# Performance work log

Hardware: AMD Instinct MI355X
Metric: run time of the kernel (lower is better)

The kernel has to match this reference:

```python
import jax, jax.numpy as jnp
import numpy as np

D_MODEL = 768
N_HEADS = 12
D_K = D_MODEL // N_HEADS


def setup_inputs() -> dict:
    key = jax.random.key(0)
    kq, kk, kv, kwq, kbq, kwo, kbo = jax.random.split(key, 7)
    B, S = 1, 4096
    s = 1.0 / np.sqrt(D_MODEL)
    return {
        "q": jax.random.normal(kq, (B, S, D_MODEL), jnp.float32),
        "k": jax.random.normal(kk, (B, S, D_MODEL), jnp.float32),
        "v": jax.random.normal(kv, (B, S, D_MODEL), jnp.float32),
        # nn.Linear weights stored as [out, in]; note the original forward
        # uses W_q for Q, K, AND V (W_k/W_v are never used), so only W_q and
        # W_o are materialized here.
        "Wq": jax.random.uniform(kwq, (D_MODEL, D_MODEL), jnp.float32, -s, s),
        "bq": jax.random.uniform(kbq, (D_MODEL,), jnp.float32, -s, s),
        "Wo": jax.random.uniform(kwo, (D_MODEL, D_MODEL), jnp.float32, -s, s),
        "bo": jax.random.uniform(kbo, (D_MODEL,), jnp.float32, -s, s),
    }


def _split_heads(x):  # [B,S,D] -> [B,H,S,Dk]
    B, S, _ = x.shape
    return x.reshape(B, S, N_HEADS, D_K).transpose(0, 2, 1, 3)


def reference(q, k, v, Wq, bq, Wo, bo):
    # Faithful to source: same W_q projection applied to q, k, v.
    Q = _split_heads(q @ Wq.T + bq)
    K = _split_heads(k @ Wq.T + bq)
    V = _split_heads(v @ Wq.T + bq)
    scale = 1.0 / np.sqrt(D_K).astype(np.float32)
    scores = jnp.einsum("bhqd,bhkd->bhqk", Q, K) * scale  # [B,H,S,S]
    probs = jax.nn.softmax(scores, axis=-1)
    atten = jnp.einsum("bhqk,bhkd->bhqd", probs, V)
    B, _, S, _ = atten.shape
    concat = atten.transpose(0, 2, 1, 3).reshape(B, S, D_MODEL)
    return concat @ Wo.T + bo
```

## Files before the change

### kernel.cpp

```cpp
#include <hip/hip_runtime.h>
#include <stdint.h>
#include <math.h>


#define SQ 4096
#define DM 768
#define NH 12

typedef float f32x4 __attribute__((ext_vector_type(4)));
typedef short bf16x8 __attribute__((ext_vector_type(8)));
typedef unsigned int u32x4 __attribute__((ext_vector_type(4)));
typedef unsigned int u32x2 __attribute__((ext_vector_type(2)));
typedef unsigned short ushort_t;

#define MFMA32(a, b, c) __builtin_amdgcn_mfma_f32_16x16x32_bf16((a), (b), (c), 0, 0, 0)

static __device__ __forceinline__ ushort_t f2bf(float f) {
    unsigned int u = __builtin_bit_cast(unsigned int, f);
    u += 0x7fffu + ((u >> 16) & 1u);
    return (ushort_t)(u >> 16);
}

static __device__ __forceinline__ unsigned int cvt_pk_bf16(float a, float b) {
    unsigned int d;
    asm("v_cvt_pk_bf16_f32 %0, %1, %2" : "=v"(d) : "v"(a), "v"(b));
    return d;
}

static __device__ __forceinline__ float exp2_hw(float x) {
    float r;
    asm("v_exp_f32 %0, %1" : "=v"(r) : "v"(x));
    return r;
}

static __device__ __forceinline__ void gload16(const ushort_t* g, ushort_t* l) {
    __builtin_amdgcn_global_load_lds(
        reinterpret_cast<const __attribute__((address_space(1))) unsigned int*>(
            reinterpret_cast<uintptr_t>(g)),
        reinterpret_cast<__attribute__((address_space(3))) unsigned int*>(
            reinterpret_cast<uintptr_t>(l)),
        16, 0, 0);
}

#define WAITV8 do { asm volatile("s_waitcnt vmcnt(8)" ::: "memory"); \
                    __builtin_amdgcn_sched_barrier(0); } while (0)
#define WAITV4 do { asm volatile("s_waitcnt vmcnt(4)" ::: "memory"); \
                    __builtin_amdgcn_sched_barrier(0); } while (0)
#define WAITV0 do { asm volatile("s_waitcnt vmcnt(0)" ::: "memory"); \
                    __builtin_amdgcn_sched_barrier(0); } while (0)
#define WAITLGKM0 do { asm volatile("s_waitcnt lgkmcnt(0)" ::: "memory"); \
                       __builtin_amdgcn_sched_barrier(0); } while (0)

__global__ __launch_bounds__(256) void cvt_all(
    const float* __restrict__ q, const float* __restrict__ k,
    const float* __restrict__ v, const float* __restrict__ Wq,
    const float* __restrict__ Wo, ushort_t* __restrict__ xb,
    ushort_t* __restrict__ wqb, ushort_t* __restrict__ wob) {
    const int NE4 = (SQ * DM) / 4;
    const int NW4 = (DM * DM) / 4;
    int i = blockIdx.x * 256 + threadIdx.x;
    const float* src;
    ushort_t* dst;
    if (i < NE4) { src = q; dst = xb; }
    else if (i < 2 * NE4) { src = k; dst = xb + SQ * DM; i -= NE4; }
    else if (i < 3 * NE4) { src = v; dst = xb + 2 * SQ * DM; i -= 2 * NE4; }
    else if (i < 3 * NE4 + NW4) { src = Wq; dst = wqb; i -= 3 * NE4; }
    else if (i < 3 * NE4 + 2 * NW4) { src = Wo; dst = wob; i -= 3 * NE4 + NW4; }
    else return;
    float4 x = reinterpret_cast<const float4*>(src)[i];
    ushort4 o;
    o.x = f2bf(x.x); o.y = f2bf(x.y); o.z = f2bf(x.z); o.w = f2bf(x.w);
    reinterpret_cast<ushort4*>(dst)[i] = o;
}

__global__ __launch_bounds__(256) void gemm_qkv(
    const ushort_t* __restrict__ xb, const ushort_t* __restrict__ wqb,
    const float* __restrict__ bq, ushort_t* __restrict__ proj,
    ushort_t* __restrict__ vt) {
    __shared__ __align__(16) ushort_t lsA[128 * 64];
    __shared__ __align__(16) ushort_t lsB[128 * 64];
    const int tid = threadIdx.x;
    const int lane = tid & 63;
    const int w = tid >> 6;
    const int wm = w >> 1, wn = w & 1;
    const int g = lane >> 4, li = lane & 15;
    const bool isV = blockIdx.x >= 384;
    const ushort_t* A;
    const ushort_t* B;
    int bm, bn;
    if (!isV) {
        A = xb; B = wqb;
        bm = blockIdx.x / 6; bn = blockIdx.x % 6;
    } else {
        A = wqb; B = xb + 2 * SQ * DM;
        const int b2 = blockIdx.x - 384;
        bm = b2 / 32; bn = b2 % 32;
    }
    const int arow = bm * 128, brow = bn * 128;
    const int sr = lane >> 3;
    const int sc = ((lane & 7) ^ sr) * 8;

    f32x4 acc[4][4] = {};

    for (int kt = 0; kt < 12; ++kt) {
        const int k0 = kt * 64;
        __syncthreads();
#pragma unroll
        for (int c = 0; c < 4; ++c) {
            const int chunk = w * 4 + c;
            const int r = chunk * 8 + sr;
            gload16(A + (size_t)(arow + r) * DM + k0 + sc, lsA + chunk * 512);
            gload16(B + (size_t)(brow + r) * DM + k0 + sc, lsB + chunk * 512);
        }
        __syncthreads();

        bf16x8 af[4][2];
#pragma unroll
        for (int mf = 0; mf < 4; ++mf) {
            const int row = wm * 64 + mf * 16 + li;
#pragma unroll
            for (int ks = 0; ks < 2; ++ks)
                af[mf][ks] = *reinterpret_cast<const bf16x8*>(
                    lsA + row * 64 + ((ks * 32 + g * 8) ^ ((li & 7) << 3)));
        }
#pragma unroll
        for (int nf = 0; nf < 4; ++nf) {
            const int row = wn * 64 + nf * 16 + li;
            bf16x8 b0 = *reinterpret_cast<const bf16x8*>(
                lsB + row * 64 + ((g * 8) ^ ((li & 7) << 3)));
            bf16x8 b1 = *reinterpret_cast<const bf16x8*>(
                lsB + row * 64 + ((32 + g * 8) ^ ((li & 7) << 3)));
#pragma unroll
            for (int mf = 0; mf < 4; ++mf) {
                acc[mf][nf] = MFMA32(af[mf][0], b0, acc[mf][nf]);
                acc[mf][nf] = MFMA32(af[mf][1], b1, acc[mf][nf]);
            }
        }
    }

    if (!isV) {
        const float qscale = (arow < 4096) ? 0.18033688011112042f : 1.0f;
#pragma unroll
        for (int nf = 0; nf < 4; ++nf) {
            const int col = brow + wn * 64 + nf * 16 + li;
            const float bv = bq[col];
#pragma unroll
            for (int mf = 0; mf < 4; ++mf) {
                const int row0 = arow + wm * 64 + mf * 16 + g * 4;
#pragma unroll
                for (int r = 0; r < 4; ++r)
                    proj[(size_t)(row0 + r) * DM + col] = f2bf((acc[mf][nf][r] + bv) * qscale);
            }
        }
    } else {
        float bv[4][4];
#pragma unroll
        for (int mf = 0; mf < 4; ++mf)
#pragma unroll
            for (int r = 0; r < 4; ++r)
                bv[mf][r] = bq[arow + wm * 64 + mf * 16 + g * 4 + r];
        const int xg = (g & 1) << 3;
#pragma unroll
        for (int nf = 0; nf < 4; ++nf) {
            const int j = brow + wn * 64 + nf * 16 + li;
            const int pos = j ^ xg;
#pragma unroll
            for (int mf = 0; mf < 4; ++mf) {
                const int row0 = arow + wm * 64 + mf * 16 + g * 4;
#pragma unroll
                for (int r = 0; r < 4; ++r)
                    vt[(size_t)(row0 + r) * SQ + pos] = f2bf(acc[mf][nf][r] + bv[mf][r]);
            }
        }
    }
}

__global__ __launch_bounds__(256) void gemm_out(
    const ushort_t* __restrict__ cc, const ushort_t* __restrict__ wob,
    const float* __restrict__ bo, float* __restrict__ outf) {
    __shared__ __align__(16) ushort_t lsA[128 * 64];
    __shared__ __align__(16) ushort_t lsB[128 * 64];
    const int tid = threadIdx.x;
    const int lane = tid & 63;
    const int w = tid >> 6;
    const int wm = w >> 1, wn = w & 1;
    const int g = lane >> 4, li = lane & 15;
    const int bm = blockIdx.x / 6, bn = blockIdx.x % 6;
    const int arow = bm * 128, brow = bn * 128;
    const int sr = lane >> 3;
    const int sc = ((lane & 7) ^ sr) * 8;

    f32x4 acc[4][4] = {};

    for (int kt = 0; kt < 12; ++kt) {
        const int k0 = kt * 64;
        __syncthreads();
#pragma unroll
        for (int c = 0; c < 4; ++c) {
            const int chunk = w * 4 + c;
            const int r = chunk * 8 + sr;
            gload16(cc + (size_t)(arow + r) * DM + k0 + sc, lsA + chunk * 512);
            gload16(wob + (size_t)(brow + r) * DM + k0 + sc, lsB + chunk * 512);
        }
        __syncthreads();

        bf16x8 af[4][2];
#pragma unroll
        for (int mf = 0; mf < 4; ++mf) {
            const int row = wm * 64 + mf * 16 + li;
#pragma unroll
            for (int ks = 0; ks < 2; ++ks)
                af[mf][ks] = *reinterpret_cast<const bf16x8*>(
                    lsA + row * 64 + ((ks * 32 + g * 8) ^ ((li & 7) << 3)));
        }
#pragma unroll
        for (int nf = 0; nf < 4; ++nf) {
            const int row = wn * 64 + nf * 16 + li;
            bf16x8 b0 = *reinterpret_cast<const bf16x8*>(
                lsB + row * 64 + ((g * 8) ^ ((li & 7) << 3)));
            bf16x8 b1 = *reinterpret_cast<const bf16x8*>(
                lsB + row * 64 + ((32 + g * 8) ^ ((li & 7) << 3)));
#pragma unroll
            for (int mf = 0; mf < 4; ++mf) {
                acc[mf][nf] = MFMA32(af[mf][0], b0, acc[mf][nf]);
                acc[mf][nf] = MFMA32(af[mf][1], b1, acc[mf][nf]);
            }
        }
    }

#pragma unroll
    for (int nf = 0; nf < 4; ++nf) {
        const int col = brow + wn * 64 + nf * 16 + li;
        const float bv = bo[col];
#pragma unroll
        for (int mf = 0; mf < 4; ++mf) {
            const int row0 = arow + wm * 64 + mf * 16 + g * 4;
#pragma unroll
            for (int r = 0; r < 4; ++r)
                outf[(size_t)(row0 + r) * DM + col] = acc[mf][nf][r] + bv;
        }
    }
}

__global__ __launch_bounds__(256, 3) void attn_bf16(
    const ushort_t* __restrict__ qk, const ushort_t* __restrict__ vtb,
    ushort_t* __restrict__ cc) {
    __shared__ __align__(16) ushort_t smem[24576];

    const int tid = threadIdx.x, lane = tid & 63, w = tid >> 6;
    const int g = lane >> 4, li = lane & 15;
    const int logical = (blockIdx.x & 7) * 96 + (blockIdx.x >> 3);
    const int h = logical >> 6, qb = logical & 63;
    const int sr = lane >> 3;
    const int sc = ((lane & 7) ^ sr) * 8;
    const int vd = lane >> 1, vh = lane & 1;

    const ushort_t* Kb = qk + (size_t)(4096 + w * 1024) * DM + (size_t)h * 64;
    const ushort_t* Vb = vtb + (size_t)(h * 64) * SQ + w * 1024;

    ushort_t* base = smem + w * 6144;
    ushort_t* K0 = base;          ushort_t* V0 = base + 1024;
    ushort_t* K1 = base + 2048;   ushort_t* V1 = base + 3072;
    ushort_t* K2 = base + 4096;   ushort_t* V2 = base + 5120;

    const int ko0 = li * 64 + ((g * 8) ^ ((li & 7) << 3));
    const int ko1 = li * 64 + ((32 + g * 8) ^ ((li & 7) << 3));
    const int vo = li * 16 + 4 * (g ^ (((li >> 2) & 1) << 1));

    bf16x8 qf[4][2];
#pragma unroll
    for (int qh = 0; qh < 4; ++qh)
#pragma unroll
        for (int ks = 0; ks < 2; ++ks)
            qf[qh][ks] = *reinterpret_cast<const bf16x8*>(
                qk + (size_t)(qb * 64 + qh * 16 + li) * DM + h * 64 + ks * 32 + g * 8);

    f32x4 oacc[4][5] = {};
    u32x2 paA[4];

    const unsigned int one2 = 0x3F803F80u;
    u32x4 onesu = {one2, one2, one2, one2};
    const bf16x8 vones = __builtin_bit_cast(bf16x8, onesu);

    auto stage = [&](ushort_t* KT, ushort_t* VT, int kvo) {
        gload16(Kb + (size_t)(kvo + sr) * DM + sc, KT);
        gload16(Kb + (size_t)(kvo + 8 + sr) * DM + sc, KT + 512);
        gload16(Vb + (size_t)vd * SQ + kvo + vh * 8, VT);
        gload16(Vb + (size_t)(32 + vd) * SQ + kvo + vh * 8, VT + 512);
    };

    auto qkexp = [&](const ushort_t* KT, f32x4* P) {
        bf16x8 kb0 = *reinterpret_cast<const bf16x8*>(KT + ko0);
        bf16x8 kb1 = *reinterpret_cast<const bf16x8*>(KT + ko1);
        __builtin_amdgcn_s_setprio(1);
#pragma unroll
        for (int qh = 0; qh < 4; ++qh) {
            f32x4 s = {};
            s = MFMA32(kb0, qf[qh][0], s);
            s = MFMA32(kb1, qf[qh][1], s);
            P[qh] = s;
        }
        __builtin_amdgcn_s_setprio(0);
#pragma unroll
        for (int qh = 0; qh < 4; ++qh) {
            f32x4 p;
#pragma unroll
            for (int r = 0; r < 4; ++r) p[r] = exp2_hw(P[qh][r]);
            P[qh] = p;
        }
    };

    auto pvacc = [&](const ushort_t* VA, const ushort_t* VB, const bf16x8* pa) {
        __builtin_amdgcn_s_setprio(1);
#pragma unroll
        for (int nv = 0; nv < 4; ++nv) {
            short4 a4 = *reinterpret_cast<const short4*>(VA + vo + nv * 256);
            short4 b4 = *reinterpret_cast<const short4*>(VB + vo + nv * 256);
            bf16x8 vb = {a4.x, a4.y, a4.z, a4.w, b4.x, b4.y, b4.z, b4.w};
#pragma unroll
            for (int qh = 0; qh < 4; ++qh)
                oacc[qh][nv] = MFMA32(pa[qh], vb, oacc[qh][nv]);
        }
#pragma unroll
        for (int qh = 0; qh < 4; ++qh)
            oacc[qh][4] = MFMA32(pa[qh], vones, oacc[qh][4]);
        __builtin_amdgcn_s_setprio(0);
    };

    auto packA = [&](const f32x4* P) {
#pragma unroll
        for (int qh = 0; qh < 4; ++qh) {
            u32x2 u;
            u.x = cvt_pk_bf16(P[qh][0], P[qh][1]);
            u.y = cvt_pk_bf16(P[qh][2], P[qh][3]);
            paA[qh] = u;
        }
    };

    auto packO = [&](const f32x4* P, bf16x8* pa) {
#pragma unroll
        for (int qh = 0; qh < 4; ++qh) {
            u32x4 pu;
            pu.x = paA[qh].x;
            pu.y = paA[qh].y;
            pu.z = cvt_pk_bf16(P[qh][0], P[qh][1]);
            pu.w = cvt_pk_bf16(P[qh][2], P[qh][3]);
            pa[qh] = __builtin_bit_cast(bf16x8, pu);
        }
    };

    auto pair_full = [&](ushort_t* KE, ushort_t* VE, ushort_t* KO, ushort_t* VO,
                         ushort_t* KS1, ushort_t* VS1, ushort_t* KS2,
                         ushort_t* VS2, int e) {
        stage(KS1, VS1, (e + 2) * 16);
        WAITV8;
        f32x4 P[4];
        qkexp(KE, P);
        packA(P);
        WAITV4;
        f32x4 P2[4];
        qkexp(KO, P2);
        bf16x8 pa[4];
        packO(P2, pa);
        pvacc(VE, VO, pa);
        WAITLGKM0;
        stage(KS2, VS2, (e + 3) * 16);
    };

    WAITV0;
    stage(K0, V0, 0);
    stage(K1, V1, 16);

#pragma unroll 1
    for (int i = 0; i < 10; ++i) {
        const int e = i * 6;
        pair_full(K0, V0, K1, V1, K2, V2, K0, V0, e);
        pair_full(K2, V2, K0, V0, K1, V1, K2, V2, e + 2);
        pair_full(K1, V1, K2, V2, K0, V0, K1, V1, e + 4);
    }
    pair_full(K0, V0, K1, V1, K2, V2, K0, V0, 60);
    {
        WAITV4;
        f32x4 P[4];
        qkexp(K2, P);
        packA(P);
        WAITV0;
        f32x4 P2[4];
        qkexp(K0, P2);
        bf16x8 pa[4];
        packO(P2, pa);
        pvacc(V2, V0, pa);
    }

    __syncthreads();
    float* ob = reinterpret_cast<float*>(smem);
    if (w >= 2) {
        float* bse = ob + (w - 2) * 5120;
#pragma unroll
        for (int qh = 0; qh < 4; ++qh)
#pragma unroll
            for (int nv = 0; nv < 5; ++nv)
                *reinterpret_cast<f32x4*>(
                    bse + ((qh * 5 + nv) * 64 + lane) * 4) = oacc[qh][nv];
    }
    __syncthreads();
    if (w < 2) {
        const float* bse = ob + w * 5120;
#pragma unroll
        for (int qh = 0; qh < 4; ++qh)
#pragma unroll
            for (int nv = 0; nv < 5; ++nv)
                oacc[qh][nv] += *reinterpret_cast<const f32x4*>(
                    bse + ((qh * 5 + nv) * 64 + lane) * 4);
    }
    __syncthreads();
    if (w == 1) {
#pragma unroll
        for (int qh = 0; qh < 4; ++qh)
#pragma unroll
            for (int nv = 0; nv < 5; ++nv)
                *reinterpret_cast<f32x4*>(
                    ob + ((qh * 5 + nv) * 64 + lane) * 4) = oacc[qh][nv];
    }
    __syncthreads();
    if (w == 0) {
#pragma unroll
        for (int qh = 0; qh < 4; ++qh)
#pragma unroll
            for (int nv = 0; nv < 5; ++nv)
                oacc[qh][nv] += *reinterpret_cast<const f32x4*>(
                    ob + ((qh * 5 + nv) * 64 + lane) * 4);
#pragma unroll
        for (int qh = 0; qh < 4; ++qh) {
            float inv[4];
#pragma unroll
            for (int r = 0; r < 4; ++r) inv[r] = 1.0f / oacc[qh][4][r];
#pragma unroll
            for (int nv = 0; nv < 4; ++nv)
#pragma unroll
                for (int r = 0; r < 4; ++r) {
                    const int row = qb * 64 + qh * 16 + g * 4 + r;
                    const int col = h * 64 + nv * 16 + li;
                    cc[(size_t)row * DM + col] = f2bf(oacc[qh][nv][r] * inv[r]);
                }
        }
    }
}

extern "C" void kernel_launch(void* const* d_in, const int* in_sizes, int n_in,
                              void* d_out, int out_size, void* d_ws, size_t ws_size,
                              hipStream_t stream) {
    const float* q = (const float*)d_in[0];
    const float* k = (const float*)d_in[1];
    const float* v = (const float*)d_in[2];
    const float* Wq = (const float*)d_in[3];
    const float* bq = (const float*)d_in[4];
    const float* Wo = (const float*)d_in[5];
    const float* bo = (const float*)d_in[6];
    float* out = (float*)d_out;

    ushort_t* ws = (ushort_t*)d_ws;
    const int NE = SQ * DM;
    ushort_t* xb = ws;
    ushort_t* wqb = ws + 3 * NE;
    ushort_t* wob = wqb + DM * DM;
    ushort_t* proj = wob + DM * DM;
    ushort_t* vt = proj + 2 * NE;
    ushort_t* cc = vt + NE;

    const int n4 = 3 * (NE / 4) + 2 * ((DM * DM) / 4);
    cvt_all<<<(n4 + 255) / 256, 256, 0, stream>>>(q, k, v, Wq, Wo, xb, wqb, wob);

    gemm_qkv<<<576, 256, 0, stream>>>(xb, wqb, bq, proj, vt);

    attn_bf16<<<NH * (SQ / 64), 256, 0, stream>>>(proj, vt, cc);

    gemm_out<<<(SQ / 128) * 6, 256, 0, stream>>>(cc, wob, bo, out);
}
```

Measured before the change: 140.5 us.

## Pre-pack K and V into MFMA fragment order and load directly to registers

Adds a relayout kernel that rewrites K and transposed V into per-lane MFMA fragment order, reusing the spent input workspace. The attention kernel then drops its LDS staging pipeline: each wave loads K/V fragments straight into registers with coalesced 16-byte loads, double-buffered in registers, and LDS is kept only for the final cross-wave reduction. The intent is to remove the LDS round trip, the manual waitcnt choreography and the bank-swizzle logic. In exchange it adds an extra kernel launch and a full pass over K/V memory, and raises register pressure under the three-blocks-per-SIMD launch bound.

```diff
diff --git a/kernel.cpp b/kernel.cpp
--- a/kernel.cpp
+++ b/kernel.cpp
@@ -10,7 +10,6 @@
 typedef float f32x4 __attribute__((ext_vector_type(4)));
 typedef short bf16x8 __attribute__((ext_vector_type(8)));
 typedef unsigned int u32x4 __attribute__((ext_vector_type(4)));
-typedef unsigned int u32x2 __attribute__((ext_vector_type(2)));
 typedef unsigned short ushort_t;
 
 #define MFMA32(a, b, c) __builtin_amdgcn_mfma_f32_16x16x32_bf16((a), (b), (c), 0, 0, 0)
@@ -41,15 +40,6 @@
             reinterpret_cast<uintptr_t>(l)),
         16, 0, 0);
 }
-
-#define WAITV8 do { asm volatile("s_waitcnt vmcnt(8)" ::: "memory"); \
-                    __builtin_amdgcn_sched_barrier(0); } while (0)
-#define WAITV4 do { asm volatile("s_waitcnt vmcnt(4)" ::: "memory"); \
-                    __builtin_amdgcn_sched_barrier(0); } while (0)
-#define WAITV0 do { asm volatile("s_waitcnt vmcnt(0)" ::: "memory"); \
-                    __builtin_amdgcn_sched_barrier(0); } while (0)
-#define WAITLGKM0 do { asm volatile("s_waitcnt lgkmcnt(0)" ::: "memory"); \
-                       __builtin_amdgcn_sched_barrier(0); } while (0)
 
 __global__ __launch_bounds__(256) void cvt_all(
     const float* __restrict__ q, const float* __restrict__ k,
@@ -159,19 +149,40 @@
 #pragma unroll
             for (int r = 0; r < 4; ++r)
                 bv[mf][r] = bq[arow + wm * 64 + mf * 16 + g * 4 + r];
-        const int xg = (g & 1) << 3;
 #pragma unroll
         for (int nf = 0; nf < 4; ++nf) {
             const int j = brow + wn * 64 + nf * 16 + li;
-            const int pos = j ^ xg;
 #pragma unroll
             for (int mf = 0; mf < 4; ++mf) {
                 const int row0 = arow + wm * 64 + mf * 16 + g * 4;
 #pragma unroll
                 for (int r = 0; r < 4; ++r)
-                    vt[(size_t)(row0 + r) * SQ + pos] = f2bf(acc[mf][nf][r] + bv[mf][r]);
+                    vt[(size_t)(row0 + r) * SQ + j] = f2bf(acc[mf][nf][r] + bv[mf][r]);
             }
         }
+    }
+}
+
+__global__ __launch_bounds__(256) void relayout(
+    const ushort_t* __restrict__ proj, const ushort_t* __restrict__ vt,
+    ushort_t* __restrict__ kpp, ushort_t* __restrict__ vpp) {
+    const int u = blockIdx.x * 256 + threadIdx.x;
+    if (u < 393216) {
+        const int l = u & 63, f = (u >> 6) & 1, t = (u >> 7) & 255, h = u >> 15;
+        const ushort_t* s = proj + (size_t)(4096 + 16 * t + (l & 15)) * DM +
+                            64 * h + 32 * f + 8 * (l >> 4);
+        *reinterpret_cast<bf16x8*>(kpp + (size_t)u * 8) =
+            *reinterpret_cast<const bf16x8*>(s);
+    } else {
+        const int u2 = u - 393216;
+        const int l = u2 & 63, nv = (u2 >> 6) & 3, p = (u2 >> 8) & 127, h = u2 >> 15;
+        const int dm = 64 * h + 16 * nv + (l & 15);
+        const int kv0 = 32 * p + 4 * (l >> 4);
+        ushort4 e = *reinterpret_cast<const ushort4*>(vt + (size_t)dm * SQ + kv0);
+        ushort4 o = *reinterpret_cast<const ushort4*>(vt + (size_t)dm * SQ + kv0 + 16);
+        ushort4* dst = reinterpret_cast<ushort4*>(vpp + (size_t)u2 * 8);
+        dst[0] = e;
+        dst[1] = o;
     }
 }
 
@@ -243,29 +254,17 @@
 }
 
 __global__ __launch_bounds__(256, 3) void attn_bf16(
-    const ushort_t* __restrict__ qk, const ushort_t* __restrict__ vtb,
-    ushort_t* __restrict__ cc) {
-    __shared__ __align__(16) ushort_t smem[24576];
+    const ushort_t* __restrict__ qk, const ushort_t* __restrict__ kpp,
+    const ushort_t* __restrict__ vpp, ushort_t* __restrict__ cc) {
+    __shared__ __align__(16) float ob[10240];
 
     const int tid = threadIdx.x, lane = tid & 63, w = tid >> 6;
     const int g = lane >> 4, li = lane & 15;
     const int logical = (blockIdx.x & 7) * 96 + (blockIdx.x >> 3);
     const int h = logical >> 6, qb = logical & 63;
-    const int sr = lane >> 3;
-    const int sc = ((lane & 7) ^ sr) * 8;
-    const int vd = lane >> 1, vh = lane & 1;
-
-    const ushort_t* Kb = qk + (size_t)(4096 + w * 1024) * DM + (size_t)h * 64;
-    const ushort_t* Vb = vtb + (size_t)(h * 64) * SQ + w * 1024;
-
-    ushort_t* base = smem + w * 6144;
-    ushort_t* K0 = base;          ushort_t* V0 = base + 1024;
-    ushort_t* K1 = base + 2048;   ushort_t* V1 = base + 3072;
-    ushort_t* K2 = base + 4096;   ushort_t* V2 = base + 5120;
-
-    const int ko0 = li * 64 + ((g * 8) ^ ((li & 7) << 3));
-    const int ko1 = li * 64 + ((32 + g * 8) ^ ((li & 7) << 3));
-    const int vo = li * 16 + 4 * (g ^ (((li >> 2) & 1) << 1));
+
+    const ushort_t* kbase = kpp + (size_t)(h * 256 + w * 64) * 1024 + lane * 8;
+    const ushort_t* vbase = vpp + (size_t)(h * 128 + w * 32) * 2048 + lane * 8;
 
     bf16x8 qf[4][2];
 #pragma unroll
@@ -276,124 +275,76 @@
                 qk + (size_t)(qb * 64 + qh * 16 + li) * DM + h * 64 + ks * 32 + g * 8);
 
     f32x4 oacc[4][5] = {};
-    u32x2 paA[4];
 
     const unsigned int one2 = 0x3F803F80u;
     u32x4 onesu = {one2, one2, one2, one2};
     const bf16x8 vones = __builtin_bit_cast(bf16x8, onesu);
 
-    auto stage = [&](ushort_t* KT, ushort_t* VT, int kvo) {
-        gload16(Kb + (size_t)(kvo + sr) * DM + sc, KT);
-        gload16(Kb + (size_t)(kvo + 8 + sr) * DM + sc, KT + 512);
-        gload16(Vb + (size_t)vd * SQ + kvo + vh * 8, VT);
-        gload16(Vb + (size_t)(32 + vd) * SQ + kvo + vh * 8, VT + 512);
-    };
-
-    auto qkexp = [&](const ushort_t* KT, f32x4* P) {
-        bf16x8 kb0 = *reinterpret_cast<const bf16x8*>(KT + ko0);
-        bf16x8 kb1 = *reinterpret_cast<const bf16x8*>(KT + ko1);
-        __builtin_amdgcn_s_setprio(1);
-#pragma unroll
-        for (int qh = 0; qh < 4; ++qh) {
-            f32x4 s = {};
-            s = MFMA32(kb0, qf[qh][0], s);
-            s = MFMA32(kb1, qf[qh][1], s);
-            P[qh] = s;
-        }
-        __builtin_amdgcn_s_setprio(0);
-#pragma unroll
-        for (int qh = 0; qh < 4; ++qh) {
-            f32x4 p;
-#pragma unroll
-            for (int r = 0; r < 4; ++r) p[r] = exp2_hw(P[qh][r]);
-            P[qh] = p;
-        }
-    };
-
-    auto pvacc = [&](const ushort_t* VA, const ushort_t* VB, const bf16x8* pa) {
-        __builtin_amdgcn_s_setprio(1);
-#pragma unroll
-        for (int nv = 0; nv < 4; ++nv) {
-            short4 a4 = *reinterpret_cast<const short4*>(VA + vo + nv * 256);
-            short4 b4 = *reinterpret_cast<const short4*>(VB + vo + nv * 256);
-            bf16x8 vb = {a4.x, a4.y, a4.z, a4.w, b4.x, b4.y, b4.z, b4.w};
-#pragma unroll
-            for (int qh = 0; qh < 4; ++qh)
-                oacc[qh][nv] = MFMA32(pa[qh], vb, oacc[qh][nv]);
-        }
-#pragma unroll
-        for (int qh = 0; qh < 4; ++qh)
-            oacc[qh][4] = MFMA32(pa[qh], vones, oacc[qh][4]);
-        __builtin_amdgcn_s_setprio(0);
-    };
-
-    auto packA = [&](const f32x4* P) {
-#pragma unroll
-        for (int qh = 0; qh < 4; ++qh) {
-            u32x2 u;
-            u.x = cvt_pk_bf16(P[qh][0], P[qh][1]);
-            u.y = cvt_pk_bf16(P[qh][2], P[qh][3]);
-            paA[qh] = u;
-        }
-    };
-
-    auto packO = [&](const f32x4* P, bf16x8* pa) {
-#pragma unroll
-        for (int qh = 0; qh < 4; ++qh) {
-            u32x4 pu;
-            pu.x = paA[qh].x;
-            pu.y = paA[qh].y;
-            pu.z = cvt_pk_bf16(P[qh][0], P[qh][1]);
-            pu.w = cvt_pk_bf16(P[qh][2], P[qh][3]);
-            pa[qh] = __builtin_bit_cast(bf16x8, pu);
-        }
-    };
-
-    auto pair_full = [&](ushort_t* KE, ushort_t* VE, ushort_t* KO, ushort_t* VO,
-                         ushort_t* KS1, ushort_t* VS1, ushort_t* KS2,
-                         ushort_t* VS2, int e) {
-        stage(KS1, VS1, (e + 2) * 16);
-        WAITV8;
-        f32x4 P[4];
-        qkexp(KE, P);
-        packA(P);
-        WAITV4;
-        f32x4 P2[4];
-        qkexp(KO, P2);
-        bf16x8 pa[4];
-        packO(P2, pa);
-        pvacc(VE, VO, pa);
-        WAITLGKM0;
-        stage(KS2, VS2, (e + 3) * 16);
-    };
-
-    WAITV0;
-    stage(K0, V0, 0);
-    stage(K1, V1, 16);
-
+#define LOADPAIR(BUF, p)                                                       \
+    do {                                                                       \
+        const ushort_t* kp_ = kbase + (size_t)(p) * 2048;                      \
+        const ushort_t* vp_ = vbase + (size_t)(p) * 2048;                      \
+        BUF[0] = *reinterpret_cast<const bf16x8*>(kp_);                        \
+        BUF[1] = *reinterpret_cast<const bf16x8*>(kp_ + 512);                  \
+        BUF[2] = *reinterpret_cast<const bf16x8*>(kp_ + 1024);                 \
+        BUF[3] = *reinterpret_cast<const bf16x8*>(kp_ + 1536);                 \
+        BUF[4] = *reinterpret_cast<const bf16x8*>(vp_);                        \
+        BUF[5] = *reinterpret_cast<const bf16x8*>(vp_ + 512);                  \
+        BUF[6] = *reinterpret_cast<const bf16x8*>(vp_ + 1024);                 \
+        BUF[7] = *reinterpret_cast<const bf16x8*>(vp_ + 1536);                 \
+    } while (0)
+
+#define COMPUTE(BUF)                                                           \
+    do {                                                                       \
+        f32x4 Pe_[4], Po_[4];                                                  \
+        __builtin_amdgcn_s_setprio(1);                                         \
+        _Pragma("unroll") for (int qh = 0; qh < 4; ++qh) {                     \
+            f32x4 s = {};                                                      \
+            s = MFMA32(BUF[0], qf[qh][0], s);                                  \
+            s = MFMA32(BUF[1], qf[qh][1], s);                                  \
+            Pe_[qh] = s;                                                       \
+        }                                                                      \
+        _Pragma("unroll") for (int qh = 0; qh < 4; ++qh) {                     \
+            f32x4 s = {};                                                      \
+            s = MFMA32(BUF[2], qf[qh][0], s);                                  \
+            s = MFMA32(BUF[3], qf[qh][1], s);                                  \
+            Po_[qh] = s;                                                       \
+        }                                                                      \
+        __builtin_amdgcn_s_setprio(0);                                         \
+        bf16x8 pa_[4];                                                         \
+        _Pragma("unroll") for (int qh = 0; qh < 4; ++qh) {                     \
+            u32x4 pu;                                                          \
+            pu.x = cvt_pk_bf16(exp2_hw(Pe_[qh][0]), exp2_hw(Pe_[qh][1]));      \
+            pu.y = cvt_pk_bf16(exp2_hw(Pe_[qh][2]), exp2_hw(Pe_[qh][3]));      \
+            pu.z = cvt_pk_bf16(exp2_hw(Po_[qh][0]), exp2_hw(Po_[qh][1]));      \
+            pu.w = cvt_pk_bf16(exp2_hw(Po_[qh][2]), exp2_hw(Po_[qh][3]));      \
+            pa_[qh] = __builtin_bit_cast(bf16x8, pu);                          \
+        }                                                                      \
+        __builtin_amdgcn_s_setprio(1);                                         \
+        _Pragma("unroll") for (int nv = 0; nv < 4; ++nv)                       \
+            _Pragma("unroll") for (int qh = 0; qh < 4; ++qh)                   \
+                oacc[qh][nv] = MFMA32(pa_[qh], BUF[4 + nv], oacc[qh][nv]);     \
+        _Pragma("unroll") for (int qh = 0; qh < 4; ++qh)                       \
+            oacc[qh][4] = MFMA32(pa_[qh], vones, oacc[qh][4]);                 \
+        __builtin_amdgcn_s_setprio(0);                                         \
+    } while (0)
+
+    bf16x8 Abuf[8], Bbuf[8];
+    LOADPAIR(Abuf, 0);
 #pragma unroll 1
-    for (int i = 0; i < 10; ++i) {
-        const int e = i * 6;
-        pair_full(K0, V0, K1, V1, K2, V2, K0, V0, e);
-        pair_full(K2, V2, K0, V0, K1, V1, K2, V2, e + 2);
-        pair_full(K1, V1, K2, V2, K0, V0, K1, V1, e + 4);
-    }
-    pair_full(K0, V0, K1, V1, K2, V2, K0, V0, 60);
-    {
-        WAITV4;
-        f32x4 P[4];
-        qkexp(K2, P);
-        packA(P);
-        WAITV0;
-        f32x4 P2[4];
-        qkexp(K0, P2);
-        bf16x8 pa[4];
-        packO(P2, pa);
-        pvacc(V2, V0, pa);
-    }
+    for (int p = 0; p < 30; p += 2) {
+        LOADPAIR(Bbuf, p + 1);
+        COMPUTE(Abuf);
+        LOADPAIR(Abuf, p + 2);
+        COMPUTE(Bbuf);
+    }
+    LOADPAIR(Bbuf, 31);
+    COMPUTE(Abuf);
+    COMPUTE(Bbuf);
+#undef LOADPAIR
+#undef COMPUTE
 
     __syncthreads();
-    float* ob = reinterpret_cast<float*>(smem);
     if (w >= 2) {
         float* bse = ob + (w - 2) * 5120;
 #pragma unroll
@@ -467,13 +418,17 @@
     ushort_t* proj = wob + DM * DM;
     ushort_t* vt = proj + 2 * NE;
     ushort_t* cc = vt + NE;
+    ushort_t* kpp = xb;
+    ushort_t* vpp = xb + NE;
 
     const int n4 = 3 * (NE / 4) + 2 * ((DM * DM) / 4);
     cvt_all<<<(n4 + 255) / 256, 256, 0, stream>>>(q, k, v, Wq, Wo, xb, wqb, wob);
 
     gemm_qkv<<<576, 256, 0, stream>>>(xb, wqb, bq, proj, vt);
 
-    attn_bf16<<<NH * (SQ / 64), 256, 0, stream>>>(proj, vt, cc);
+    relayout<<<3072, 256, 0, stream>>>(proj, vt, kpp, vpp);
+
+    attn_bf16<<<NH * (SQ / 64), 256, 0, stream>>>(proj, kpp, vpp, cc);
 
     gemm_out<<<(SQ / 128) * 6, 256, 0, stream>>>(cc, wob, bo, out);
 }
```

Measured after the change: 323.6 us. 2.3x slower.
